# Performance work log

Hardware: AMD Instinct MI355X
Metric: run time of the kernel (lower is better)

## Reference

```python
import jax, jax.numpy as jnp
import numpy as np

OUT_H, OUT_W = 7, 7
SPATIAL_SCALE = 0.0625
N_IMG, C, H, W = 2, 256, 38, 38
NUM_ROIS = 256
IMG_MAX = 607.9  # keeps floor(coord*scale) <= 37


def setup_inputs() -> dict:
    key = jax.random.key(0)
    k_feat, k_b, k_xa, k_xb, k_ya, k_yb = jax.random.split(key, 6)
    feat = jax.random.normal(k_feat, (N_IMG, C, H, W), dtype=jnp.float32)
    bidx = jax.random.randint(k_b, (NUM_ROIS,), 0, N_IMG).astype(jnp.float32)
    xa = jax.random.uniform(k_xa, (NUM_ROIS,), minval=0.0, maxval=IMG_MAX)
    xb = jax.random.uniform(k_xb, (NUM_ROIS,), minval=0.0, maxval=IMG_MAX)
    ya = jax.random.uniform(k_ya, (NUM_ROIS,), minval=0.0, maxval=IMG_MAX)
    yb = jax.random.uniform(k_yb, (NUM_ROIS,), minval=0.0, maxval=IMG_MAX)
    rois = jnp.stack([bidx,
                      jnp.minimum(xa, xb), jnp.minimum(ya, yb),
                      jnp.maximum(xa, xb), jnp.maximum(ya, yb)], axis=1)
    return {"input": feat, "rois": rois.astype(jnp.float32)}


def _roi_max_pool(feat_all, rois):
    # feat_all: (N, C, H, W); rois: (R, 5) = (batch_idx, x1, y1, x2, y2)
    H_, W_ = feat_all.shape[2], feat_all.shape[3]
    b = rois[:, 0].astype(jnp.int32)
    # torch: rois[:,1:].mul_(scale); rois.long() -> truncation (== floor for >=0)
    coords = jnp.floor(rois[:, 1:] * SPATIAL_SCALE).astype(jnp.int32)
    x1, y1, x2, y2 = coords[:, 0], coords[:, 1], coords[:, 2], coords[:, 3]
    rh = y2 - y1 + 1  # inclusive crop: [y1, y2+1)
    rw = x2 - x1 + 1
    feat = feat_all[b]  # (R, C, H, W) per-ROI gather of its image
    neg = jnp.array(-jnp.inf, feat.dtype)

    # separable adaptive max pool: rows then cols
    hs = jnp.arange(H_)
    rows = []
    for i in range(OUT_H):  # fixed small loop over output bins
        hstart = y1 + (i * rh) // OUT_H                       # floor(i*rh/OUT_H)
        hend = y1 + ((i + 1) * rh + OUT_H - 1) // OUT_H       # ceil
        m = (hs[None, :] >= hstart[:, None]) & (hs[None, :] < hend[:, None])  # (R,H)
        rows.append(jnp.max(jnp.where(m[:, None, :, None], feat, neg), axis=2))  # (R,C,W)
    rowmax = jnp.stack(rows, axis=2)  # (R, C, OUT_H, W)

    ws = jnp.arange(W_)
    cols = []
    for j in range(OUT_W):
        wstart = x1 + (j * rw) // OUT_W
        wend = x1 + ((j + 1) * rw + OUT_W - 1) // OUT_W
        m = (ws[None, :] >= wstart[:, None]) & (ws[None, :] < wend[:, None])  # (R,W)
        cols.append(jnp.max(jnp.where(m[:, None, None, :], rowmax, neg), axis=3))  # (R,C,OUT_H)
    return jnp.stack(cols, axis=3)  # (R, C, OUT_H, OUT_W)


def reference(input, rois):
    return _roi_max_pool(input, rois)
```

## Files before the change

kernel.cpp:

```cpp
#include <hip/hip_runtime.h>
#include <math.h>

#define OUT_H 7
#define OUT_W 7
#define N_C 256
#define FH 38
#define FW 38
#define NUM_ROIS 256
#define SPATIAL_SCALE 0.0625f

__global__ __launch_bounds__(256) void roi_pool_kernel(
    const float* __restrict__ feat,
    const float* __restrict__ rois,
    float* __restrict__ out)
{
    int t = blockIdx.x * blockDim.x + threadIdx.x;

    int j = t % OUT_W;
    int i = (t / OUT_W) % OUT_H;
    int c = (t / (OUT_W * OUT_H)) % N_C;
    int r = t / (OUT_W * OUT_H * N_C);

    const float* roi = rois + r * 5;
    int b  = (int)roi[0];
    int x1 = (int)(roi[1] * SPATIAL_SCALE);
    int y1 = (int)(roi[2] * SPATIAL_SCALE);
    int x2 = (int)(roi[3] * SPATIAL_SCALE);
    int y2 = (int)(roi[4] * SPATIAL_SCALE);
    int rh = y2 - y1 + 1;
    int rw = x2 - x1 + 1;

    int hstart = y1 + (i * rh) / OUT_H;
    int hend   = y1 + ((i + 1) * rh + OUT_H - 1) / OUT_H;
    int wstart = x1 + (j * rw) / OUT_W;
    int wend   = x1 + ((j + 1) * rw + OUT_W - 1) / OUT_W;

    const float* fp = feat + ((size_t)b * N_C + c) * (FH * FW);
    float m = -INFINITY;
    for (int h = hstart; h < hend; ++h) {
        const float* row = fp + h * FW;
        for (int w = wstart; w < wend; ++w) {
            m = fmaxf(m, row[w]);
        }
    }
    out[t] = m;
}

extern "C" void kernel_launch(void* const* d_in, const int* in_sizes, int n_in,
                              void* d_out, int out_size, void* d_ws, size_t ws_size,
                              hipStream_t stream) {
    const float* feat = (const float*)d_in[0];
    const float* rois = (const float*)d_in[1];
    float* out = (float*)d_out;

    int total = NUM_ROIS * N_C * OUT_H * OUT_W;
    int block = 256;
    int grid = (total + block - 1) / block;
    roi_pool_kernel<<<grid, block, 0, stream>>>(feat, rois, out);
}
```

Baseline: 79.89 us.

## Use one wavefront per ROI-channel with separable row-then-column max via LDS

Each 64-lane wavefront now handles one (ROI, channel) plane. Lanes take the ROI's columns, reduce over rows for each of the seven output rows with coalesced loads, and store column maxima in shared memory. A second phase reduces across columns to produce the 49 outputs. This replaces the per-output-element loop, which read overlapping windows with scattered accesses, with separable pooling that reads each element once. In exchange it adds a block-wide barrier and leaves lanes idle when the ROI is narrow.

```diff
diff --git a/kernel.cpp b/kernel.cpp
--- a/kernel.cpp
+++ b/kernel.cpp
@@ -9,41 +9,55 @@
 #define NUM_ROIS 256
 #define SPATIAL_SCALE 0.0625f
 
-__global__ __launch_bounds__(256) void roi_pool_kernel(
+__global__ __launch_bounds__(256) void roi_pool_wave(
     const float* __restrict__ feat,
     const float* __restrict__ rois,
     float* __restrict__ out)
 {
-    int t = blockIdx.x * blockDim.x + threadIdx.x;
+    __shared__ float cmax[4][OUT_H][64];
 
-    int j = t % OUT_W;
-    int i = (t / OUT_W) % OUT_H;
-    int c = (t / (OUT_W * OUT_H)) % N_C;
-    int r = t / (OUT_W * OUT_H * N_C);
+    const int lane = threadIdx.x & 63;
+    const int wv   = threadIdx.x >> 6;
+    const int g    = blockIdx.x * 4 + wv;
+    const int r    = g >> 8;
+    const int c    = g & 255;
 
     const float* roi = rois + r * 5;
-    int b  = (int)roi[0];
-    int x1 = (int)(roi[1] * SPATIAL_SCALE);
-    int y1 = (int)(roi[2] * SPATIAL_SCALE);
-    int x2 = (int)(roi[3] * SPATIAL_SCALE);
-    int y2 = (int)(roi[4] * SPATIAL_SCALE);
-    int rh = y2 - y1 + 1;
-    int rw = x2 - x1 + 1;
+    const int b  = (int)roi[0];
+    const int x1 = (int)(roi[1] * SPATIAL_SCALE);
+    const int y1 = (int)(roi[2] * SPATIAL_SCALE);
+    const int x2 = (int)(roi[3] * SPATIAL_SCALE);
+    const int y2 = (int)(roi[4] * SPATIAL_SCALE);
+    const int rh = y2 - y1 + 1;
+    const int rw = x2 - x1 + 1;
 
-    int hstart = y1 + (i * rh) / OUT_H;
-    int hend   = y1 + ((i + 1) * rh + OUT_H - 1) / OUT_H;
-    int wstart = x1 + (j * rw) / OUT_W;
-    int wend   = x1 + ((j + 1) * rw + OUT_W - 1) / OUT_W;
+    const float* plane   = feat + ((size_t)(b * N_C + c)) * (FH * FW);
+    const float* colbase = plane + x1 + lane;
+    const bool   active  = lane < rw;
 
-    const float* fp = feat + ((size_t)b * N_C + c) * (FH * FW);
-    float m = -INFINITY;
-    for (int h = hstart; h < hend; ++h) {
-        const float* row = fp + h * FW;
-        for (int w = wstart; w < wend; ++w) {
-            m = fmaxf(m, row[w]);
+    #pragma unroll
+    for (int i = 0; i < OUT_H; ++i) {
+        const int hs = y1 + (i * rh) / OUT_H;
+        const int he = y1 + ((i + 1) * rh + OUT_H - 1) / OUT_H;
+        float m = -INFINITY;
+        if (active) {
+            for (int h = hs; h < he; ++h)
+                m = fmaxf(m, colbase[h * FW]);
         }
+        cmax[wv][i][lane] = m;
     }
-    out[t] = m;
+    __syncthreads();
+
+    if (lane < OUT_H * OUT_W) {
+        const int i = lane / OUT_W;
+        const int j = lane % OUT_W;
+        const int ws = (j * rw) / OUT_W;
+        const int we = ((j + 1) * rw + OUT_W - 1) / OUT_W;
+        float o = -INFINITY;
+        for (int t = ws; t < we; ++t)
+            o = fmaxf(o, cmax[wv][i][t]);
+        out[((size_t)(r * N_C + c)) * (OUT_H * OUT_W) + lane] = o;
+    }
 }
 
 extern "C" void kernel_launch(void* const* d_in, const int* in_sizes, int n_in,
@@ -53,8 +67,6 @@
     const float* rois = (const float*)d_in[1];
     float* out = (float*)d_out;
 
-    int total = NUM_ROIS * N_C * OUT_H * OUT_W;
-    int block = 256;
-    int grid = (total + block - 1) / block;
-    roi_pool_kernel<<<grid, block, 0, stream>>>(feat, rois, out);
+    const int grid = (NUM_ROIS * N_C) / 4;
+    roi_pool_wave<<<grid, 256, 0, stream>>>(feat, rois, out);
 }
```

After: 100.5 us. +25.8%, slower.
